# Kernel optimization log

Hardware: AMD Instinct MI355X
Metric: run time of the kernel (lower is better)

Reference implementation:

```python
import jax, jax.numpy as jnp
from jax import lax
import numpy as np

NUM_INST = 32   # upper bound on instance ids (segment count)
B, H, W = 2, 512, 1024
FM = 16         # featuremap_count (hard-coded in module)
DS = 4          # downsample_count
DN = ('NCHW', 'OIHW', 'NCHW')
EPS = 1e-5


def conv(x, w, b, stride, pad, reflect=False):
    if reflect:
        x = jnp.pad(x, ((0, 0), (0, 0), (pad, pad), (pad, pad)), mode='reflect')
        padding = 'VALID'
    else:
        padding = ((pad, pad), (pad, pad))
    y = lax.conv_general_dilated(x, w, (stride, stride), padding, dimension_numbers=DN)
    return y + b[None, :, None, None]


def conv_transpose(x, w, b):
    # PyTorch ConvTranspose2d(k=3, s=2, p=1, output_padding=1) == dilated conv with
    # flipped kernel, lhs_dilation=2, asymmetric padding (1, 2) -> output 2*H
    wr = w[:, :, ::-1, ::-1]
    y = lax.conv_general_dilated(x, wr, (1, 1), ((1, 2), (1, 2)),
                                 lhs_dilation=(2, 2), dimension_numbers=DN)
    return y + b[None, :, None, None]


def instance_norm(x):
    mu = jnp.mean(x, axis=(2, 3), keepdims=True)
    var = jnp.var(x, axis=(2, 3), keepdims=True)
    return (x - mu) * lax.rsqrt(var + EPS)


def average_pool(x, inst):
    # Per-image, per-instance mean over pixels, broadcast back (segment mean).
    Bq, C, Hq, Wq = x.shape
    ids = inst[:, 0].reshape(Bq, Hq * Wq)       # [B, HW] int segment ids
    flat = x.reshape(Bq, C, Hq * Wq)

    def per_image(xf, idf):                      # xf: [C, HW], idf: [HW]
        sums = jax.ops.segment_sum(xf.T, idf, num_segments=NUM_INST)   # [NUM_INST, C]
        cnts = jax.ops.segment_sum(jnp.ones_like(idf, xf.dtype), idf,
                                   num_segments=NUM_INST)              # [NUM_INST]
        means = sums / jnp.maximum(cnts, 1.0)[:, None]
        return means[idf].T                      # gather mean back to pixels [C, HW]

    return jax.vmap(per_image)(flat, ids).reshape(Bq, C, Hq, Wq)


def setup_inputs() -> dict:
    key = jax.random.key(0)
    ks = iter(jax.random.split(key, 64))
    inp = {}
    inp['input_tensor'] = jax.random.normal(next(ks), (B, 3, H, W), jnp.float32)
    inp['instance_map'] = jax.random.randint(next(ks), (B, 1, H, W), 0, NUM_INST)

    def wb(cout, cin, k):
        w = jax.random.normal(next(ks), (cout, cin, k, k), jnp.float32) / np.sqrt(cin * k * k)
        b = jax.random.normal(next(ks), (cout,), jnp.float32) * 0.01
        return w, b

    chans = [FM * 2 ** i for i in range(DS + 1)]  # 16, 32, 64, 128, 256
    inp['e0_w'], inp['e0_b'] = wb(FM, 3, 7)
    for i in range(DS):
        inp[f'e{i + 1}_w'], inp[f'e{i + 1}_b'] = wb(chans[i + 1], chans[i], 3)
    for i in range(DS):
        inp[f'd{i}_w'], inp[f'd{i}_b'] = wb(chans[DS - i - 1], chans[DS - i], 3)
    inp['d4_w'], inp['d4_b'] = wb(3, FM, 7)
    return inp


def reference(input_tensor, instance_map,
              e0_w, e0_b, e1_w, e1_b, e2_w, e2_b, e3_w, e3_b, e4_w, e4_b,
              d0_w, d0_b, d1_w, d1_b, d2_w, d2_b, d3_w, d3_b, d4_w, d4_b):
    # Encoder: reflect-pad 7x7 conv then 4 stride-2 downsampling convs (IN + ReLU)
    x = jax.nn.relu(instance_norm(conv(input_tensor, e0_w, e0_b, 1, 3, reflect=True)))
    for w, b in ((e1_w, e1_b), (e2_w, e2_b), (e3_w, e3_b), (e4_w, e4_b)):
        x = jax.nn.relu(instance_norm(conv(x, w, b, 2, 1)))
    # Decoder: 4 stride-2 transpose convs (IN + ReLU), final reflect-pad 7x7 conv (no norm/relu)
    for w, b in ((d0_w, d0_b), (d1_w, d1_b), (d2_w, d2_b), (d3_w, d3_b)):
        x = jax.nn.relu(instance_norm(conv_transpose(x, w, b)))
    x = conv(x, d4_w, d4_b, 1, 3, reflect=True)
    x = jnp.tanh(x)
    return average_pool(x, instance_map)
```

## Files before the change

kernel.cpp:

```cpp
#include <hip/hip_runtime.h>
#include <cstddef>

#define NUM_INST 32
#define EPS_IN 1e-5f

__device__ __forceinline__ int reflect_idx(int i, int n) {
    if (i < 0) i = -i;
    else if (i >= n) i = 2 * n - 2 - i;
    return i;
}

__device__ __forceinline__ float tanh_fast(float v) {
    float a = fminf(fmaxf(v, -9.f), 9.f);
    float e = __expf(2.f * a);
    return (e - 1.f) / (e + 1.f);
}

template<int CIN, int COUT>
__global__ void __launch_bounds__(256, 4)
conv7_l0(const float* __restrict__ x, const float* __restrict__ w,
         const float* __restrict__ bias, float* __restrict__ y, int H, int W)
{
    __shared__ float wsm[CIN * 49 * COUT];
    __shared__ float tile[CIN][38 * 23];
    const int tid = threadIdx.x;
    const int b = blockIdx.z;

    for (int idx = tid; idx < CIN * 49 * COUT; idx += 256) {
        int oc = idx % COUT;
        int r  = idx / COUT;
        wsm[idx] = w[(size_t)oc * CIN * 49 + r];
    }
    const int oh_base = blockIdx.y * 32, ow_base = blockIdx.x * 16;
    for (int idx = tid; idx < CIN * 38 * 22; idx += 256) {
        int c  = idx / (38 * 22);
        int rr = idx % (38 * 22);
        int r  = rr / 22, col = rr % 22;
        int gy = reflect_idx(oh_base - 3 + r, H);
        int gx = reflect_idx(ow_base - 3 + col, W);
        tile[c][r * 23 + col] = x[((size_t)(b * CIN + c)) * H * W + (size_t)gy * W + gx];
    }
    __syncthreads();

    const int row = tid >> 3;
    const int col2 = (tid & 7) * 2;

    float acc[2][COUT];
#pragma unroll
    for (int o = 0; o < COUT; ++o) {
        float bv = bias[o];
        acc[0][o] = bv; acc[1][o] = bv;
    }

#pragma unroll
    for (int ic = 0; ic < CIN; ++ic) {
        const float* tp = &tile[ic][0];
        const float4* wp4 = (const float4*)&wsm[ic * 49 * COUT];
#pragma unroll
        for (int kh = 0; kh < 7; ++kh) {
            float rv[8];
#pragma unroll
            for (int i = 0; i < 8; ++i) rv[i] = tp[(row + kh) * 23 + col2 + i];
#pragma unroll
            for (int kw = 0; kw < 7; ++kw) {
#pragma unroll
                for (int o4 = 0; o4 < COUT / 4; ++o4) {
                    float4 wv = wp4[(kh * 7 + kw) * (COUT / 4) + o4];
                    acc[0][o4 * 4 + 0] += rv[kw] * wv.x;
                    acc[0][o4 * 4 + 1] += rv[kw] * wv.y;
                    acc[0][o4 * 4 + 2] += rv[kw] * wv.z;
                    acc[0][o4 * 4 + 3] += rv[kw] * wv.w;
                    acc[1][o4 * 4 + 0] += rv[kw + 1] * wv.x;
                    acc[1][o4 * 4 + 1] += rv[kw + 1] * wv.y;
                    acc[1][o4 * 4 + 2] += rv[kw + 1] * wv.z;
                    acc[1][o4 * 4 + 3] += rv[kw + 1] * wv.w;
                }
            }
        }
    }

    const int oh = oh_base + row, ow0 = ow_base + col2;
#pragma unroll
    for (int o = 0; o < COUT; ++o) {
        float2 st;
        st.x = acc[0][o]; st.y = acc[1][o];
        *(float2*)&y[(((size_t)b * COUT + o) * H + oh) * W + ow0] = st;
    }
}

template<int CIN, int NCH>
__global__ void __launch_bounds__(256, 4)
conv7_seg(const float* __restrict__ x, const float* __restrict__ w,
          const float* __restrict__ bias,
          const float* __restrict__ mu, const float* __restrict__ rs,
          const int* __restrict__ inst, float* __restrict__ seg, int H, int W)
{
    __shared__ float wsm[CIN * 49 * 4];
    __shared__ float tile[NCH][38 * 39];
    __shared__ float smu[CIN], srs[CIN];
    __shared__ float ls[NUM_INST * 4];
    const int tid = threadIdx.x;
    const int b = blockIdx.z;

    if (tid < NUM_INST * 4) ls[tid] = 0.f;
    for (int idx = tid; idx < CIN * 49 * 4; idx += 256) {
        int ocp = idx & 3;
        int r   = idx >> 2;
        wsm[idx] = (ocp < 3) ? w[(size_t)ocp * CIN * 49 + r] : 0.f;
    }
    if (tid < CIN) { smu[tid] = mu[b * CIN + tid]; srs[tid] = rs[b * CIN + tid]; }

    const int oh_base = blockIdx.y * 32, ow_base = blockIdx.x * 32;
    const int row = tid >> 3;
    const int col4 = (tid & 7) * 4;

    float acc[4][3];
#pragma unroll
    for (int c = 0; c < 3; ++c) {
        float bv = bias[c];
#pragma unroll
        for (int j = 0; j < 4; ++j) acc[j][c] = bv;
    }

    for (int ic0 = 0; ic0 < CIN; ic0 += NCH) {
        __syncthreads();
        for (int idx = tid; idx < NCH * 38 * 38; idx += 256) {
            int c  = idx / (38 * 38);
            int rr = idx % (38 * 38);
            int r  = rr / 38, cl = rr % 38;
            int gy = reflect_idx(oh_base - 3 + r, H);
            int gx = reflect_idx(ow_base - 3 + cl, W);
            int ic = ic0 + c;
            float v = x[((size_t)(b * CIN + ic)) * H * W + (size_t)gy * W + gx];
            v = fmaxf((v - smu[ic]) * srs[ic], 0.f);
            tile[c][r * 39 + cl] = v;
        }
        __syncthreads();
#pragma unroll
        for (int cc = 0; cc < NCH; ++cc) {
            const float* tp = &tile[cc][0];
            const float4* wp4 = (const float4*)&wsm[(ic0 + cc) * 49 * 4];
#pragma unroll
            for (int kh = 0; kh < 7; ++kh) {
                float rv[10];
#pragma unroll
                for (int i = 0; i < 10; ++i) rv[i] = tp[(row + kh) * 39 + col4 + i];
#pragma unroll
                for (int kw = 0; kw < 7; ++kw) {
                    float4 wv = wp4[kh * 7 + kw];
#pragma unroll
                    for (int j = 0; j < 4; ++j) {
                        acc[j][0] += rv[kw + j] * wv.x;
                        acc[j][1] += rv[kw + j] * wv.y;
                        acc[j][2] += rv[kw + j] * wv.z;
                    }
                }
            }
        }
    }

    const int oh = oh_base + row, ow0 = ow_base + col4;
    const int* ip = inst + (size_t)b * H * W + (size_t)oh * W + ow0;
    int4 ia = *(const int4*)ip;
    int idv[4] = {ia.x, ia.y, ia.z, ia.w};
#pragma unroll
    for (int j = 0; j < 4; ++j) {
        int base = idv[j] * 4;
        atomicAdd(&ls[base + 0], tanh_fast(acc[j][0]));
        atomicAdd(&ls[base + 1], tanh_fast(acc[j][1]));
        atomicAdd(&ls[base + 2], tanh_fast(acc[j][2]));
        atomicAdd(&ls[base + 3], 1.f);
    }
    __syncthreads();
    if (tid < NUM_INST * 4)
        atomicAdd(&seg[b * NUM_INST * 4 + tid], ls[tid]);
}

template<int CIN, int COUT, int OCPT, int KS, bool NORM>
__global__ void __launch_bounds__(256)
conv3_s2(const float* __restrict__ x, const float* __restrict__ w,
         const float* __restrict__ bias,
         const float* __restrict__ mu, const float* __restrict__ rs,
         float* __restrict__ y, size_t ystride, int Hin, int Win)
{
    const int Hout = Hin >> 1, Wout = Win >> 1;
    constexpr int CK = CIN / KS;
    __shared__ float wsm[CK * 9 * OCPT];
    __shared__ float smu[CIN], srs[CIN];
    const int tid = threadIdx.x;
    const int NG = COUT / OCPT;
    const int z = blockIdx.z;
    const int ks = z % KS;
    const int ogb = z / KS;
    const int b = ogb / NG, g = ogb % NG;
    const int oc0 = g * OCPT;
    const int icbase = ks * CK;
    for (int idx = tid; idx < CK * 9 * OCPT; idx += 256) {
        int o = idx % OCPT;
        int r = idx / OCPT;
        wsm[idx] = w[(size_t)(oc0 + o) * CIN * 9 + (size_t)icbase * 9 + r];
    }
    if (NORM && tid < CIN) { smu[tid] = mu[b * CIN + tid]; srs[tid] = rs[b * CIN + tid]; }
    __syncthreads();

    const int ow = blockIdx.x * 16 + (tid & 15);
    const int oh = blockIdx.y * 16 + (tid >> 4);

    float acc[OCPT];
#pragma unroll
    for (int o = 0; o < OCPT; ++o) acc[o] = (ks == 0) ? bias[oc0 + o] : 0.f;

    for (int icl = 0; icl < CK; ++icl) {
        const int ic = icbase + icl;
        const float* xp = x + ((size_t)(b * CIN + ic)) * Hin * Win;
        float m = NORM ? smu[ic] : 0.f;
        float rr = NORM ? srs[ic] : 0.f;
#pragma unroll
        for (int kh = 0; kh < 3; ++kh) {
            int ih = 2 * oh + kh - 1;
            if (ih < 0 || ih >= Hin) continue;
#pragma unroll
            for (int kw = 0; kw < 3; ++kw) {
                int iw = 2 * ow + kw - 1;
                if (iw < 0 || iw >= Win) continue;
                float v = xp[(size_t)ih * Win + iw];
                if (NORM) v = fmaxf((v - m) * rr, 0.f);
                const float* wp = &wsm[(icl * 9 + kh * 3 + kw) * OCPT];
#pragma unroll
                for (int o = 0; o < OCPT; ++o) acc[o] += wp[o] * v;
            }
        }
    }
    float* yb = y + (size_t)ks * ystride;
    float* yp = yb + (((size_t)b * COUT + oc0) * Hout + oh) * Wout + ow;
#pragma unroll
    for (int o = 0; o < OCPT; ++o) yp[(size_t)o * Hout * Wout] = acc[o];
}

template<int CIN, int COUT, int ICB, int KS>
__global__ void __launch_bounds__(256)
tconv3_v2(const float* __restrict__ x, const float* __restrict__ w,
          const float* __restrict__ bias,
          const float* __restrict__ mu, const float* __restrict__ rs,
          float* __restrict__ y, size_t ystride, int Hin, int Win)
{
    constexpr int OCB = 16;
    constexpr int NOG = COUT / OCB;
    constexpr int CK = CIN / KS;
    const int z = blockIdx.z;
    const int ks = z % KS;
    const int ogb = z / KS;
    const int b = ogb / NOG;
    const int ocb = (ogb % NOG) * OCB;
    const int r0 = blockIdx.y * 8, c0 = blockIdx.x * 32;
    const int Hout = Hin * 2, Wout = Win * 2;

    __shared__ float xt[ICB][9 * 36];
    __shared__ float wt[ICB][9][OCB];
    __shared__ float smu[CIN], srs[CIN];

    const int tid = threadIdx.x;
    if (tid < CIN) { smu[tid] = mu[b * CIN + tid]; srs[tid] = rs[b * CIN + tid]; }

    const int tid_s = tid & 63;
    const int og = tid >> 6;
    const int sr = tid_s >> 3;
    const int sc4 = (tid_s & 7) * 4;

    float acc[4][4][4];
#pragma unroll
    for (int o = 0; o < 4; ++o) {
        float bv = (ks == 0) ? bias[ocb + og * 4 + o] : 0.f;
#pragma unroll
        for (int pr = 0; pr < 4; ++pr)
#pragma unroll
            for (int p = 0; p < 4; ++p) acc[pr][o][p] = bv;
    }

    for (int ic0 = ks * CK; ic0 < (ks + 1) * CK; ic0 += ICB) {
        __syncthreads();
        for (int idx = tid; idx < ICB * 9 * 33; idx += 256) {
            int c  = idx / (9 * 33);
            int rr = idx % (9 * 33);
            int r  = rr / 33, col = rr % 33;
            int gr = r0 + r, gc = c0 + col;
            int ic = ic0 + c;
            float v = 0.f;
            if (gr < Hin && gc < Win) {
                v = x[((size_t)(b * CIN + ic)) * Hin * Win + (size_t)gr * Win + gc];
                v = fmaxf((v - smu[ic]) * srs[ic], 0.f);
            }
            xt[c][r * 36 + col] = v;
        }
        for (int idx = tid; idx < ICB * 9 * OCB; idx += 256) {
            int oc  = idx & (OCB - 1);
            int tap = (idx >> 4) % 9;
            int c   = idx / (9 * OCB);
            wt[c][tap][oc] = w[(size_t)(ocb + oc) * CIN * 9 + (size_t)(ic0 + c) * 9 + tap];
        }
        __syncthreads();

#pragma unroll 4
        for (int c = 0; c < ICB; ++c) {
            const float* xr = &xt[c][sr * 36 + sc4];
            float x0[5], x1[5];
            {
                float4 a = *(const float4*)xr;
                x0[0] = a.x; x0[1] = a.y; x0[2] = a.z; x0[3] = a.w; x0[4] = xr[4];
                float4 bq = *(const float4*)(xr + 36);
                x1[0] = bq.x; x1[1] = bq.y; x1[2] = bq.z; x1[3] = bq.w; x1[4] = xr[40];
            }
            const float* wp = &wt[c][0][og * 4];
#define TAPFMA(TAP, PAR, XV, SH)                                                   \
            {                                                                      \
                float4 wq = *(const float4*)(wp + (TAP) * OCB);                    \
                float wv[4] = {wq.x, wq.y, wq.z, wq.w};                            \
                _Pragma("unroll")                                                  \
                for (int o = 0; o < 4; ++o)                                        \
                    _Pragma("unroll")                                              \
                    for (int p = 0; p < 4; ++p)                                    \
                        acc[PAR][o][p] += wv[o] * XV[p + SH];                      \
            }
            TAPFMA(4, 0, x0, 0)
            TAPFMA(5, 1, x0, 0)
            TAPFMA(3, 1, x0, 1)
            TAPFMA(7, 2, x0, 0)
            TAPFMA(1, 2, x1, 0)
            TAPFMA(8, 3, x0, 0)
            TAPFMA(6, 3, x0, 1)
            TAPFMA(2, 3, x1, 0)
            TAPFMA(0, 3, x1, 1)
#undef TAPFMA
        }
    }

    float* yb = y + (size_t)ks * ystride;
    const int gr = r0 + sr, gc = c0 + sc4;
#pragma unroll
    for (int o = 0; o < 4; ++o) {
        int oc = ocb + og * 4 + o;
        float* yp = yb + (((size_t)(b * COUT + oc)) * Hout + 2 * gr) * Wout + 2 * gc;
        float4 e0, e1, d0, d1;
        e0.x = acc[0][o][0]; e0.y = acc[1][o][0]; e0.z = acc[0][o][1]; e0.w = acc[1][o][1];
        e1.x = acc[0][o][2]; e1.y = acc[1][o][2]; e1.z = acc[0][o][3]; e1.w = acc[1][o][3];
        d0.x = acc[2][o][0]; d0.y = acc[3][o][0]; d0.z = acc[2][o][1]; d0.w = acc[3][o][1];
        d1.x = acc[2][o][2]; d1.y = acc[3][o][2]; d1.z = acc[2][o][3]; d1.w = acc[3][o][3];
        *(float4*)yp = e0;
        *(float4*)(yp + 4) = e1;
        *(float4*)(yp + Wout) = d0;
        *(float4*)(yp + Wout + 4) = d1;
    }
}

template<int KS>
__global__ void __launch_bounds__(256)
reduce_stats(const float* __restrict__ parts, size_t pstride,
             float* __restrict__ out, float* __restrict__ acc, int HW)
{
    const int bc = blockIdx.x;
    const int chunk = HW / gridDim.y;
    const size_t base = (size_t)bc * HW + (size_t)blockIdx.y * chunk;
    float s = 0.f, ss = 0.f;
    const int n4 = chunk >> 2;
    for (int i = threadIdx.x; i < n4; i += 256) {
        float4 v = ((const float4*)(parts + base))[i];
#pragma unroll
        for (int k = 1; k < KS; ++k) {
            float4 u = ((const float4*)(parts + (size_t)k * pstride + base))[i];
            v.x += u.x; v.y += u.y; v.z += u.z; v.w += u.w;
        }
        ((float4*)(out + base))[i] = v;
        s += v.x + v.y + v.z + v.w;
        ss += v.x * v.x + v.y * v.y + v.z * v.z + v.w * v.w;
    }
#pragma unroll
    for (int off = 32; off; off >>= 1) {
        s += __shfl_down(s, off);
        ss += __shfl_down(ss, off);
    }
    __shared__ float rbuf[8];
    const int wid = threadIdx.x >> 6;
    if ((threadIdx.x & 63) == 0) { rbuf[wid] = s; rbuf[4 + wid] = ss; }
    __syncthreads();
    if (threadIdx.x == 0) {
        s = rbuf[0] + rbuf[1] + rbuf[2] + rbuf[3];
        ss = rbuf[4] + rbuf[5] + rbuf[6] + rbuf[7];
        atomicAdd(&acc[bc], s);
        atomicAdd(&acc[512 + bc], ss);
    }
}

__global__ void __launch_bounds__(256)
in_stats_partial(const float* __restrict__ y, float* __restrict__ acc, int HW)
{
    const int bc = blockIdx.x;
    const int chunk = HW / gridDim.y;
    const float* p = y + (size_t)bc * HW + (size_t)blockIdx.y * chunk;
    float s = 0.f, ss = 0.f;
    const float4* p4 = (const float4*)p;
    const int n4 = chunk >> 2;
    for (int i = threadIdx.x; i < n4; i += 256) {
        float4 v = p4[i];
        s += v.x + v.y + v.z + v.w;
        ss += v.x * v.x + v.y * v.y + v.z * v.z + v.w * v.w;
    }
#pragma unroll
    for (int off = 32; off; off >>= 1) {
        s += __shfl_down(s, off);
        ss += __shfl_down(ss, off);
    }
    __shared__ float rbuf[8];
    const int wid = threadIdx.x >> 6;
    if ((threadIdx.x & 63) == 0) { rbuf[wid] = s; rbuf[4 + wid] = ss; }
    __syncthreads();
    if (threadIdx.x == 0) {
        s = rbuf[0] + rbuf[1] + rbuf[2] + rbuf[3];
        ss = rbuf[4] + rbuf[5] + rbuf[6] + rbuf[7];
        atomicAdd(&acc[bc], s);
        atomicAdd(&acc[512 + bc], ss);
    }
}

__global__ void in_stats_final(const float* __restrict__ acc,
                               float* __restrict__ mu, float* __restrict__ rs,
                               int BC, float invHW)
{
    int i = blockIdx.x * 256 + threadIdx.x;
    if (i < BC) {
        float m = acc[i] * invHW;
        float var = fmaxf(acc[512 + i] * invHW - m * m, 0.f);
        mu[i] = m;
        rs[i] = rsqrtf(var + EPS_IN);
    }
}

__global__ void zero_ws_k(float* __restrict__ p, int n)
{
    int i = blockIdx.x * 256 + threadIdx.x;
    if (i < n) p[i] = 0.f;
}

__global__ void seg_means_k(const float* __restrict__ seg, float* __restrict__ means)
{
    int i = threadIdx.x;
    if (i < 2 * NUM_INST * 3) {
        int bi = i / 3, c = i % 3;
        float cnt = seg[bi * 4 + 3];
        means[i] = seg[bi * 4 + c] / fmaxf(cnt, 1.f);
    }
}

__global__ void __launch_bounds__(256)
seg_scatter(const int* __restrict__ inst, const float* __restrict__ means,
            float* __restrict__ out, int HW)
{
    const int b = blockIdx.y;
    for (int i = blockIdx.x * 256 + threadIdx.x; i < HW; i += gridDim.x * 256) {
        int id = inst[(size_t)b * HW + i];
        const float* m = &means[(b * NUM_INST + id) * 3];
        out[((size_t)b * 3 + 0) * HW + i] = m[0];
        out[((size_t)b * 3 + 1) * HW + i] = m[1];
        out[((size_t)b * 3 + 2) * HW + i] = m[2];
    }
}

extern "C" void kernel_launch(void* const* d_in, const int* in_sizes, int n_in,
                              void* d_out, int out_size, void* d_ws, size_t ws_size,
                              hipStream_t stream)
{
    const float* x_in = (const float*)d_in[0];
    const int* inst = (const int*)d_in[1];
    const float* e0w = (const float*)d_in[2];  const float* e0b = (const float*)d_in[3];
    const float* e1w = (const float*)d_in[4];  const float* e1b = (const float*)d_in[5];
    const float* e2w = (const float*)d_in[6];  const float* e2b = (const float*)d_in[7];
    const float* e3w = (const float*)d_in[8];  const float* e3b = (const float*)d_in[9];
    const float* e4w = (const float*)d_in[10]; const float* e4b = (const float*)d_in[11];
    const float* d0w = (const float*)d_in[12]; const float* d0b = (const float*)d_in[13];
    const float* d1w = (const float*)d_in[14]; const float* d1b = (const float*)d_in[15];
    const float* d2w = (const float*)d_in[16]; const float* d2b = (const float*)d_in[17];
    const float* d3w = (const float*)d_in[18]; const float* d3b = (const float*)d_in[19];
    const float* d4w = (const float*)d_in[20]; const float* d4b = (const float*)d_in[21];
    float* outp = (float*)d_out;

    float* bufA = (float*)d_ws;
    float* bufB = bufA + 16777216;
    float* st   = bufB + 8388608;
    float* acc  = st + 9 * 1024;
    float* seg  = acc + 9 * 1024;
    float* means = seg + 2 * NUM_INST * 4;

    const dim3 blk(256);
    const int H = 512, W = 1024;

    {
        int nz = 9 * 1024 + 2 * NUM_INST * 4;
        zero_ws_k<<<dim3((nz + 255) / 256), blk, 0, stream>>>(acc, nz);
    }

#define STATS(buf, L, C, HWv)                                                        \
    in_stats_partial<<<dim3(2 * (C), 8), blk, 0, stream>>>((buf), acc + (L) * 1024, (HWv)); \
    in_stats_final<<<dim3(2), blk, 0, stream>>>(acc + (L) * 1024, st + (L) * 1024,          \
                                                st + (L) * 1024 + 512, 2 * (C),             \
                                                1.0f / (HWv));

    conv7_l0<3, 16><<<dim3(W / 16, H / 32, 2), blk, 0, stream>>>(
        x_in, e0w, e0b, bufA, H, W);
    STATS(bufA, 0, 16, H * W);

    conv3_s2<16, 32, 16, 1, true><<<dim3(32, 16, 2 * 2), blk, 0, stream>>>(
        bufA, e1w, e1b, st + 0 * 1024, st + 0 * 1024 + 512, bufB, 0, 512, 1024);
    STATS(bufB, 1, 32, 256 * 512);

    conv3_s2<32, 64, 16, 1, true><<<dim3(16, 8, 2 * 4), blk, 0, stream>>>(
        bufB, e2w, e2b, st + 1 * 1024, st + 1 * 1024 + 512, bufA, 0, 256, 512);
    STATS(bufA, 2, 64, 128 * 256);

    {
        const size_t PS = 2097152;
        float* parts = bufB + 2097152;
        conv3_s2<64, 128, 16, 2, true><<<dim3(8, 4, 2 * 8 * 2), blk, 0, stream>>>(
            bufA, e3w, e3b, st + 2 * 1024, st + 2 * 1024 + 512, parts, PS, 128, 256);
        reduce_stats<2><<<dim3(2 * 128, 8), blk, 0, stream>>>(
            parts, PS, bufB, acc + 3 * 1024, 64 * 128);
        in_stats_final<<<dim3(2), blk, 0, stream>>>(acc + 3 * 1024, st + 3 * 1024,
                                                    st + 3 * 1024 + 512, 2 * 128,
                                                    1.0f / (64 * 128));
    }

    {
        const size_t PS = 1048576;
        float* parts = bufA + 1048576;
        conv3_s2<128, 256, 16, 4, true><<<dim3(4, 2, 2 * 16 * 4), blk, 0, stream>>>(
            bufB, e4w, e4b, st + 3 * 1024, st + 3 * 1024 + 512, parts, PS, 64, 128);
        reduce_stats<4><<<dim3(2 * 256, 8), blk, 0, stream>>>(
            parts, PS, bufA, acc + 4 * 1024, 32 * 64);
        in_stats_final<<<dim3(2), blk, 0, stream>>>(acc + 4 * 1024, st + 4 * 1024,
                                                    st + 4 * 1024 + 512, 2 * 256,
                                                    1.0f / (32 * 64));
    }

    {
        const size_t PS = 2097152;
        float* parts = bufA + 2097152;
        tconv3_v2<256, 128, 16, 4><<<dim3(2, 4, 2 * 8 * 4), blk, 0, stream>>>(
            bufA, d0w, d0b, st + 4 * 1024, st + 4 * 1024 + 512, parts, PS, 32, 64);
        reduce_stats<4><<<dim3(2 * 128, 8), blk, 0, stream>>>(
            parts, PS, bufB, acc + 5 * 1024, 64 * 128);
        in_stats_final<<<dim3(2), blk, 0, stream>>>(acc + 5 * 1024, st + 5 * 1024,
                                                    st + 5 * 1024 + 512, 2 * 128,
                                                    1.0f / (64 * 128));
    }

    {
        const size_t PS = 4194304;
        float* parts = bufA + 8388608;
        tconv3_v2<128, 64, 16, 2><<<dim3(4, 8, 2 * 4 * 2), blk, 0, stream>>>(
            bufB, d1w, d1b, st + 5 * 1024, st + 5 * 1024 + 512, parts, PS, 64, 128);
        reduce_stats<2><<<dim3(2 * 64, 8), blk, 0, stream>>>(
            parts, PS, bufA, acc + 6 * 1024, 128 * 256);
        in_stats_final<<<dim3(2), blk, 0, stream>>>(acc + 6 * 1024, st + 6 * 1024,
                                                    st + 6 * 1024 + 512, 2 * 64,
                                                    1.0f / (128 * 256));
    }

    tconv3_v2<64, 32, 16, 1><<<dim3(8, 16, 2 * 2), blk, 0, stream>>>(
        bufA, d2w, d2b, st + 6 * 1024, st + 6 * 1024 + 512, bufB, 0, 128, 256);
    STATS(bufB, 7, 32, 256 * 512);

    tconv3_v2<32, 16, 16, 1><<<dim3(16, 32, 2), blk, 0, stream>>>(
        bufB, d3w, d3b, st + 7 * 1024, st + 7 * 1024 + 512, bufA, 0, 256, 512);
    STATS(bufA, 8, 16, H * W);

    conv7_seg<16, 2><<<dim3(W / 32, H / 32, 2), blk, 0, stream>>>(
        bufA, d4w, d4b, st + 8 * 1024, st + 8 * 1024 + 512, inst, seg, H, W);

    seg_means_k<<<dim3(1), blk, 0, stream>>>(seg, means);
    seg_scatter<<<dim3(512, 2), blk, 0, stream>>>(inst, means, outp, H * W);

#undef STATS
}
```

Measured before the change: 968.6 us.

## Split final 7x7 conv over input channels and defer segment reduction

The final 7x7 conv is split into two input-channel halves across the grid z dimension, doubling block count. Each half writes partial outputs to a scratch buffer, and a new kernel sums the partials, applies tanh and does the per-instance segment accumulation. This aims to raise occupancy and parallelism in the heavy last conv. The cost is extra global traffic for writing and rereading about 6M floats plus one more launch. The #undef STATS line is also removed.

```diff
diff --git a/kernel.cpp b/kernel.cpp
--- a/kernel.cpp
+++ b/kernel.cpp
@@ -88,25 +88,27 @@
     }
 }
 
-template<int CIN, int NCH>
+template<int CIN, int NCH, int KS>
 __global__ void __launch_bounds__(256, 4)
-conv7_seg(const float* __restrict__ x, const float* __restrict__ w,
-          const float* __restrict__ bias,
-          const float* __restrict__ mu, const float* __restrict__ rs,
-          const int* __restrict__ inst, float* __restrict__ seg, int H, int W)
-{
-    __shared__ float wsm[CIN * 49 * 4];
+conv7_part(const float* __restrict__ x, const float* __restrict__ w,
+           const float* __restrict__ bias,
+           const float* __restrict__ mu, const float* __restrict__ rs,
+           float* __restrict__ parts, size_t pstride, int H, int W)
+{
+    constexpr int CK = CIN / KS;
+    __shared__ float wsm[CK * 49 * 4];
     __shared__ float tile[NCH][38 * 39];
     __shared__ float smu[CIN], srs[CIN];
-    __shared__ float ls[NUM_INST * 4];
     const int tid = threadIdx.x;
-    const int b = blockIdx.z;
-
-    if (tid < NUM_INST * 4) ls[tid] = 0.f;
-    for (int idx = tid; idx < CIN * 49 * 4; idx += 256) {
+    const int z = blockIdx.z;
+    const int ks = z % KS;
+    const int b = z / KS;
+    const int icbase = ks * CK;
+
+    for (int idx = tid; idx < CK * 49 * 4; idx += 256) {
         int ocp = idx & 3;
         int r   = idx >> 2;
-        wsm[idx] = (ocp < 3) ? w[(size_t)ocp * CIN * 49 + r] : 0.f;
+        wsm[idx] = (ocp < 3) ? w[(size_t)ocp * CIN * 49 + (size_t)icbase * 49 + r] : 0.f;
     }
     if (tid < CIN) { smu[tid] = mu[b * CIN + tid]; srs[tid] = rs[b * CIN + tid]; }
 
@@ -117,12 +119,12 @@
     float acc[4][3];
 #pragma unroll
     for (int c = 0; c < 3; ++c) {
-        float bv = bias[c];
+        float bv = (ks == 0) ? bias[c] : 0.f;
 #pragma unroll
         for (int j = 0; j < 4; ++j) acc[j][c] = bv;
     }
 
-    for (int ic0 = 0; ic0 < CIN; ic0 += NCH) {
+    for (int lic0 = 0; lic0 < CK; lic0 += NCH) {
         __syncthreads();
         for (int idx = tid; idx < NCH * 38 * 38; idx += 256) {
             int c  = idx / (38 * 38);
@@ -130,7 +132,7 @@
             int r  = rr / 38, cl = rr % 38;
             int gy = reflect_idx(oh_base - 3 + r, H);
             int gx = reflect_idx(ow_base - 3 + cl, W);
-            int ic = ic0 + c;
+            int ic = icbase + lic0 + c;
             float v = x[((size_t)(b * CIN + ic)) * H * W + (size_t)gy * W + gx];
             v = fmaxf((v - smu[ic]) * srs[ic], 0.f);
             tile[c][r * 39 + cl] = v;
@@ -139,7 +141,7 @@
 #pragma unroll
         for (int cc = 0; cc < NCH; ++cc) {
             const float* tp = &tile[cc][0];
-            const float4* wp4 = (const float4*)&wsm[(ic0 + cc) * 49 * 4];
+            const float4* wp4 = (const float4*)&wsm[(lic0 + cc) * 49 * 4];
 #pragma unroll
             for (int kh = 0; kh < 7; ++kh) {
                 float rv[10];
@@ -160,20 +162,46 @@
     }
 
     const int oh = oh_base + row, ow0 = ow_base + col4;
-    const int* ip = inst + (size_t)b * H * W + (size_t)oh * W + ow0;
-    int4 ia = *(const int4*)ip;
-    int idv[4] = {ia.x, ia.y, ia.z, ia.w};
-#pragma unroll
-    for (int j = 0; j < 4; ++j) {
-        int base = idv[j] * 4;
-        atomicAdd(&ls[base + 0], tanh_fast(acc[j][0]));
-        atomicAdd(&ls[base + 1], tanh_fast(acc[j][1]));
-        atomicAdd(&ls[base + 2], tanh_fast(acc[j][2]));
-        atomicAdd(&ls[base + 3], 1.f);
-    }
+    float* pb = parts + (size_t)ks * pstride;
+#pragma unroll
+    for (int c = 0; c < 3; ++c) {
+        float4 st;
+        st.x = acc[0][c]; st.y = acc[1][c]; st.z = acc[2][c]; st.w = acc[3][c];
+        *(float4*)&pb[(((size_t)b * 3 + c) * H + oh) * W + ow0] = st;
+    }
+}
+
+template<int KS>
+__global__ void __launch_bounds__(256)
+seg_final(const float* __restrict__ parts, size_t pstride,
+          const int* __restrict__ inst, float* __restrict__ seg, int HW)
+{
+    const int b = blockIdx.y;
+    __shared__ float ls[NUM_INST * 4];
+    if (threadIdx.x < NUM_INST * 4) ls[threadIdx.x] = 0.f;
     __syncthreads();
-    if (tid < NUM_INST * 4)
-        atomicAdd(&seg[b * NUM_INST * 4 + tid], ls[tid]);
+    const float* p0 = parts + (size_t)b * 3 * HW;
+    const int* ip = inst + (size_t)b * HW;
+    for (int i = blockIdx.x * 256 + threadIdx.x; i < HW; i += gridDim.x * 256) {
+        int id = ip[i];
+        float v0 = p0[i];
+        float v1 = p0[(size_t)HW + i];
+        float v2 = p0[2 * (size_t)HW + i];
+#pragma unroll
+        for (int k = 1; k < KS; ++k) {
+            const float* pk = p0 + (size_t)k * pstride;
+            v0 += pk[i];
+            v1 += pk[(size_t)HW + i];
+            v2 += pk[2 * (size_t)HW + i];
+        }
+        atomicAdd(&ls[id * 4 + 0], tanh_fast(v0));
+        atomicAdd(&ls[id * 4 + 1], tanh_fast(v1));
+        atomicAdd(&ls[id * 4 + 2], tanh_fast(v2));
+        atomicAdd(&ls[id * 4 + 3], 1.f);
+    }
+    __syncthreads();
+    if (threadIdx.x < NUM_INST * 4)
+        atomicAdd(&seg[b * NUM_INST * 4 + threadIdx.x], ls[threadIdx.x]);
 }
 
 template<int CIN, int COUT, int OCPT, int KS, bool NORM>
@@ -571,11 +599,13 @@
         bufB, d3w, d3b, st + 7 * 1024, st + 7 * 1024 + 512, bufA, 0, 256, 512);
     STATS(bufA, 8, 16, H * W);
 
-    conv7_seg<16, 2><<<dim3(W / 32, H / 32, 2), blk, 0, stream>>>(
-        bufA, d4w, d4b, st + 8 * 1024, st + 8 * 1024 + 512, inst, seg, H, W);
+    {
+        const size_t PS = 3145728;
+        conv7_part<16, 2, 2><<<dim3(W / 32, H / 32, 2 * 2), blk, 0, stream>>>(
+            bufA, d4w, d4b, st + 8 * 1024, st + 8 * 1024 + 512, bufB, PS, H, W);
+        seg_final<2><<<dim3(256, 2), blk, 0, stream>>>(bufB, PS, inst, seg, H * W);
+    }
 
     seg_means_k<<<dim3(1), blk, 0, stream>>>(seg, means);
     seg_scatter<<<dim3(512, 2), blk, 0, stream>>>(inst, means, outp, H * W);
-
-#undef STATS
-}
+}
```

Measured after the change: 972.5 us. Within noise of the previous version (+0.4%).
